# Kernel optimization log

Hardware: AMD Instinct MI355X
Metric: run time of the kernel (lower is better)

## Reference

```python
import jax, jax.numpy as jnp
import numpy as np

N_VARS = 524288      # number of input variables
WIDTH = 524288       # output width of every layer (csr[-1]+1)
FANIN = 8            # children per output node -> unrolled csr = repeat(arange(WIDTH), FANIN)
N_LAYERS = 8         # alternating SumLayer (even, log-prod) / LogSumLayer (odd, log-sum)
N_EDGES = WIDTH * FANIN
EPS = 1e-15          # epsilon used by _logsumexp_scatter_reduce (torch.full init + scatter_add)
CUTOFF = -float(np.log(2.0))


def log1mexp(x):
    # numerically accurate log(1 - exp(x)) for x < 0 (eps=0 as in forward default)
    return jnp.where(x > CUTOFF, jnp.log(-jnp.expm1(x)), jnp.log1p(-jnp.exp(x)))


def setup_inputs() -> dict:
    key = jax.random.key(0)
    ks = jax.random.split(key, 1 + N_LAYERS)
    # weights are log-probabilities: log(u), u in (0.01, 0.99)
    u = jax.random.uniform(ks[0], (N_VARS,), minval=0.01, maxval=0.99, dtype=jnp.float32)
    weights = jnp.log(u)
    in0 = 2 + 2 * N_VARS  # size of encode_input output
    ptr_list = [jax.random.randint(ks[1], (N_EDGES,), 0, in0, dtype=jnp.int32)]
    for i in range(1, N_LAYERS):
        ptr_list.append(jax.random.randint(ks[1 + i], (N_EDGES,), 0, WIDTH, dtype=jnp.int32))
    ptrs = jnp.stack(ptr_list)                                   # [L, E]
    csr = jnp.repeat(jnp.arange(WIDTH, dtype=jnp.int32), FANIN)  # unrolled CSR segment ids
    csrs = jnp.broadcast_to(csr, (N_LAYERS, N_EDGES))            # [L, E]
    return {"weights": weights, "ptrs": ptrs, "csrs": csrs}


def _forward(weights, ptrs, csrs):
    # encode_input: [zero, one, w0, neg_w0, w1, neg_w1, ...]; log semiring: zero=-inf, one=0
    neg = log1mexp(weights)
    consts = jnp.array([-jnp.inf, 0.0], dtype=weights.dtype)
    x = jnp.concatenate([consts, jnp.stack([weights, neg], axis=1).ravel()])
    for i in range(N_LAYERS):
        g = x[ptrs[i]]            # gather: x[self.ptrs]
        seg = csrs[i]
        if i % 2 == 0:
            # SumLayer: scatter_reduce 'sum' over CSR segments (log-space product)
            x = jax.ops.segment_sum(g, seg, num_segments=WIDTH)
        else:
            # LogSumLayer: stabilized scatter-logsumexp
            m = jax.lax.stop_gradient(jax.ops.segment_max(g, seg, num_segments=WIDTH))
            y = jnp.nan_to_num(g - m[seg], nan=0.0, posinf=jnp.inf, neginf=-jnp.inf)
            s = jax.ops.segment_sum(jnp.exp(y), seg, num_segments=WIDTH) + EPS
            x = jnp.log(s) + m
    return x


def reference(weights, ptrs, csrs):
    return _forward(weights, ptrs, csrs)
```

## Files before the change

### kernel.cpp

```cpp
#include <hip/hip_runtime.h>
#include <math.h>

#define NVARS   524288
#define WIDTH   524288
#define FANIN   8
#define NEDGES  (WIDTH * FANIN)
#define ENC_PAD 1048592

#define TPB     256
#define OPT     2
#define NBLK    (WIDTH / (TPB * OPT))
#define HALF    (WIDTH / 2)

typedef int v4i __attribute__((ext_vector_type(4)));

__device__ __forceinline__ v4i nt_load4(const int* p) {
    return __builtin_nontemporal_load((const v4i*)p);
}

__device__ __forceinline__ float encode_neg(float wi) {
    return (wi > -0.69314718055994530942f) ? logf(-expm1f(wi))
                                           : log1pf(-expf(wi));
}

__global__ __launch_bounds__(256) void encode_kernel(const float* __restrict__ w,
                                                     float* __restrict__ x) {
    int i = blockIdx.x * blockDim.x + threadIdx.x;
    if (i == 0) { x[0] = -__builtin_inff(); x[1] = 0.0f; }
    if (i < NVARS) {
        float wi = w[i];
        x[2 + 2 * i] = wi;
        x[3 + 2 * i] = encode_neg(wi);
    }
}

template <int IS_LSE>
__global__ __launch_bounds__(256) void layer_kernel(const int* __restrict__ ptr,
                                                    const float* __restrict__ x,
                                                    float* __restrict__ y) {
    const int tid = blockIdx.x * blockDim.x + threadIdx.x;
    const int i0 = tid;
    const int i1 = tid + HALF;

    v4i a0 = nt_load4(ptr + 8 * (size_t)i0);
    v4i b0 = nt_load4(ptr + 8 * (size_t)i0 + 4);
    v4i a1 = nt_load4(ptr + 8 * (size_t)i1);
    v4i b1 = nt_load4(ptr + 8 * (size_t)i1 + 4);

    float g0 = x[a0.x], g1 = x[a0.y], g2 = x[a0.z], g3 = x[a0.w];
    float g4 = x[b0.x], g5 = x[b0.y], g6 = x[b0.z], g7 = x[b0.w];
    float h0 = x[a1.x], h1 = x[a1.y], h2 = x[a1.z], h3 = x[a1.w];
    float h4 = x[b1.x], h5 = x[b1.y], h6 = x[b1.z], h7 = x[b1.w];

    float r0, r1;
    if (IS_LSE) {
        float m0 = fmaxf(fmaxf(fmaxf(g0, g1), fmaxf(g2, g3)),
                         fmaxf(fmaxf(g4, g5), fmaxf(g6, g7)));
        float m1 = fmaxf(fmaxf(fmaxf(h0, h1), fmaxf(h2, h3)),
                         fmaxf(fmaxf(h4, h5), fmaxf(h6, h7)));
        if (m0 == -__builtin_inff()) {
            r0 = -__builtin_inff();
        } else {
            float s0 = (__expf(g0 - m0) + __expf(g1 - m0))
                     + (__expf(g2 - m0) + __expf(g3 - m0))
                     + (__expf(g4 - m0) + __expf(g5 - m0))
                     + (__expf(g6 - m0) + __expf(g7 - m0)) + 1e-15f;
            r0 = __logf(s0) + m0;
        }
        if (m1 == -__builtin_inff()) {
            r1 = -__builtin_inff();
        } else {
            float s1 = (__expf(h0 - m1) + __expf(h1 - m1))
                     + (__expf(h2 - m1) + __expf(h3 - m1))
                     + (__expf(h4 - m1) + __expf(h5 - m1))
                     + (__expf(h6 - m1) + __expf(h7 - m1)) + 1e-15f;
            r1 = __logf(s1) + m1;
        }
    } else {
        r0 = ((g0 + g1) + (g2 + g3)) + ((g4 + g5) + (g6 + g7));
        r1 = ((h0 + h1) + (h2 + h3)) + ((h4 + h5) + (h6 + h7));
    }

    y[i0] = r0;
    y[i1] = r1;
}

extern "C" void kernel_launch(void* const* d_in, const int* in_sizes, int n_in,
                              void* d_out, int out_size, void* d_ws, size_t ws_size,
                              hipStream_t stream) {
    const float* w    = (const float*)d_in[0];
    const int*   ptrs = (const int*)d_in[1];
    float* out = (float*)d_out;
    float* ws  = (float*)d_ws;

    float* enc  = ws;
    float* bufA = ws + ENC_PAD;
    float* bufB = bufA + WIDTH;

    encode_kernel<<<NVARS / 256, 256, 0, stream>>>(w, enc);

    layer_kernel<0><<<NBLK, TPB, 0, stream>>>(ptrs + (size_t)0 * NEDGES, enc,  bufA);
    layer_kernel<1><<<NBLK, TPB, 0, stream>>>(ptrs + (size_t)1 * NEDGES, bufA, bufB);
    layer_kernel<0><<<NBLK, TPB, 0, stream>>>(ptrs + (size_t)2 * NEDGES, bufB, bufA);
    layer_kernel<1><<<NBLK, TPB, 0, stream>>>(ptrs + (size_t)3 * NEDGES, bufA, bufB);
    layer_kernel<0><<<NBLK, TPB, 0, stream>>>(ptrs + (size_t)4 * NEDGES, bufB, bufA);
    layer_kernel<1><<<NBLK, TPB, 0, stream>>>(ptrs + (size_t)5 * NEDGES, bufA, bufB);
    layer_kernel<0><<<NBLK, TPB, 0, stream>>>(ptrs + (size_t)6 * NEDGES, bufB, bufA);
    layer_kernel<1><<<NBLK, TPB, 0, stream>>>(ptrs + (size_t)7 * NEDGES, bufA, out);
}
```

Measured before the change: 186.6 us.

## Prefetch gather source into cache with coalesced loads, one output per thread

Each block now issues coalesced vector loads over a slice of the input array before its random gathers, so that collectively the whole source vector gets pulled into cache. The aim is to turn scattered DRAM misses into cache hits. The kernel also goes back to one output per thread with twice as many blocks, and the LSE branch becomes a branchless select. This adds extra streaming reads of the source vector and relies on cache residency across blocks.

```diff
diff --git a/kernel.cpp b/kernel.cpp
--- a/kernel.cpp
+++ b/kernel.cpp
@@ -8,9 +8,7 @@
 #define ENC_PAD 1048592
 
 #define TPB     256
-#define OPT     2
-#define NBLK    (WIDTH / (TPB * OPT))
-#define HALF    (WIDTH / 2)
+#define NBLK    (WIDTH / TPB)
 
 typedef int v4i __attribute__((ext_vector_type(4)));
 
@@ -34,55 +32,46 @@
     }
 }
 
-template <int IS_LSE>
+template <int IS_LSE, int PREF>
 __global__ __launch_bounds__(256) void layer_kernel(const int* __restrict__ ptr,
                                                     const float* __restrict__ x,
                                                     float* __restrict__ y) {
-    const int tid = blockIdx.x * blockDim.x + threadIdx.x;
-    const int i0 = tid;
-    const int i1 = tid + HALF;
+    const int i = blockIdx.x * blockDim.x + threadIdx.x;
 
-    v4i a0 = nt_load4(ptr + 8 * (size_t)i0);
-    v4i b0 = nt_load4(ptr + 8 * (size_t)i0 + 4);
-    v4i a1 = nt_load4(ptr + 8 * (size_t)i1);
-    v4i b1 = nt_load4(ptr + 8 * (size_t)i1 + 4);
+    v4i a = nt_load4(ptr + 8 * (size_t)i);
+    v4i b = nt_load4(ptr + 8 * (size_t)i + 4);
 
-    float g0 = x[a0.x], g1 = x[a0.y], g2 = x[a0.z], g3 = x[a0.w];
-    float g4 = x[b0.x], g5 = x[b0.y], g6 = x[b0.z], g7 = x[b0.w];
-    float h0 = x[a1.x], h1 = x[a1.y], h2 = x[a1.z], h3 = x[a1.w];
-    float h4 = x[b1.x], h5 = x[b1.y], h6 = x[b1.z], h7 = x[b1.w];
-
-    float r0, r1;
-    if (IS_LSE) {
-        float m0 = fmaxf(fmaxf(fmaxf(g0, g1), fmaxf(g2, g3)),
-                         fmaxf(fmaxf(g4, g5), fmaxf(g6, g7)));
-        float m1 = fmaxf(fmaxf(fmaxf(h0, h1), fmaxf(h2, h3)),
-                         fmaxf(fmaxf(h4, h5), fmaxf(h6, h7)));
-        if (m0 == -__builtin_inff()) {
-            r0 = -__builtin_inff();
-        } else {
-            float s0 = (__expf(g0 - m0) + __expf(g1 - m0))
-                     + (__expf(g2 - m0) + __expf(g3 - m0))
-                     + (__expf(g4 - m0) + __expf(g5 - m0))
-                     + (__expf(g6 - m0) + __expf(g7 - m0)) + 1e-15f;
-            r0 = __logf(s0) + m0;
+    int keep = 0;
+    if (PREF > 0) {
+        const v4i* src = (const v4i*)x
+                       + (size_t)(blockIdx.x >> 3) * (PREF * TPB)
+                       + threadIdx.x;
+        #pragma unroll
+        for (int k = 0; k < PREF; ++k) {
+            v4i p = src[k * TPB];
+            keep |= p.x | p.y | p.z | p.w;
         }
-        if (m1 == -__builtin_inff()) {
-            r1 = -__builtin_inff();
-        } else {
-            float s1 = (__expf(h0 - m1) + __expf(h1 - m1))
-                     + (__expf(h2 - m1) + __expf(h3 - m1))
-                     + (__expf(h4 - m1) + __expf(h5 - m1))
-                     + (__expf(h6 - m1) + __expf(h7 - m1)) + 1e-15f;
-            r1 = __logf(s1) + m1;
-        }
-    } else {
-        r0 = ((g0 + g1) + (g2 + g3)) + ((g4 + g5) + (g6 + g7));
-        r1 = ((h0 + h1) + (h2 + h3)) + ((h4 + h5) + (h6 + h7));
     }
 
-    y[i0] = r0;
-    y[i1] = r1;
+    float g0 = x[a.x], g1 = x[a.y], g2 = x[a.z], g3 = x[a.w];
+    float g4 = x[b.x], g5 = x[b.y], g6 = x[b.z], g7 = x[b.w];
+
+    float r;
+    if (IS_LSE) {
+        float m = fmaxf(fmaxf(fmaxf(g0, g1), fmaxf(g2, g3)),
+                        fmaxf(fmaxf(g4, g5), fmaxf(g6, g7)));
+        float s = (__expf(g0 - m) + __expf(g1 - m))
+                + (__expf(g2 - m) + __expf(g3 - m))
+                + (__expf(g4 - m) + __expf(g5 - m))
+                + (__expf(g6 - m) + __expf(g7 - m)) + 1e-15f;
+        float lse = __logf(s) + m;
+        r = (m == -__builtin_inff()) ? -__builtin_inff() : lse;
+    } else {
+        r = ((g0 + g1) + (g2 + g3)) + ((g4 + g5) + (g6 + g7));
+    }
+
+    y[i] = r;
+    asm volatile("" :: "v"(keep));
 }
 
 extern "C" void kernel_launch(void* const* d_in, const int* in_sizes, int n_in,
@@ -99,12 +88,12 @@
 
     encode_kernel<<<NVARS / 256, 256, 0, stream>>>(w, enc);
 
-    layer_kernel<0><<<NBLK, TPB, 0, stream>>>(ptrs + (size_t)0 * NEDGES, enc,  bufA);
-    layer_kernel<1><<<NBLK, TPB, 0, stream>>>(ptrs + (size_t)1 * NEDGES, bufA, bufB);
-    layer_kernel<0><<<NBLK, TPB, 0, stream>>>(ptrs + (size_t)2 * NEDGES, bufB, bufA);
-    layer_kernel<1><<<NBLK, TPB, 0, stream>>>(ptrs + (size_t)3 * NEDGES, bufA, bufB);
-    layer_kernel<0><<<NBLK, TPB, 0, stream>>>(ptrs + (size_t)4 * NEDGES, bufB, bufA);
-    layer_kernel<1><<<NBLK, TPB, 0, stream>>>(ptrs + (size_t)5 * NEDGES, bufA, bufB);
-    layer_kernel<0><<<NBLK, TPB, 0, stream>>>(ptrs + (size_t)6 * NEDGES, bufB, bufA);
-    layer_kernel<1><<<NBLK, TPB, 0, stream>>>(ptrs + (size_t)7 * NEDGES, bufA, out);
+    layer_kernel<0, 4><<<NBLK, TPB, 0, stream>>>(ptrs + (size_t)0 * NEDGES, enc,  bufA);
+    layer_kernel<1, 2><<<NBLK, TPB, 0, stream>>>(ptrs + (size_t)1 * NEDGES, bufA, bufB);
+    layer_kernel<0, 2><<<NBLK, TPB, 0, stream>>>(ptrs + (size_t)2 * NEDGES, bufB, bufA);
+    layer_kernel<1, 2><<<NBLK, TPB, 0, stream>>>(ptrs + (size_t)3 * NEDGES, bufA, bufB);
+    layer_kernel<0, 2><<<NBLK, TPB, 0, stream>>>(ptrs + (size_t)4 * NEDGES, bufB, bufA);
+    layer_kernel<1, 2><<<NBLK, TPB, 0, stream>>>(ptrs + (size_t)5 * NEDGES, bufA, bufB);
+    layer_kernel<0, 2><<<NBLK, TPB, 0, stream>>>(ptrs + (size_t)6 * NEDGES, bufB, bufA);
+    layer_kernel<1, 2><<<NBLK, TPB, 0, stream>>>(ptrs + (size_t)7 * NEDGES, bufA, out);
 }
```

New measurement: 191.2 us. +2.5%, slower.
